# Kernel optimization log

Hardware: AMD Instinct MI355X
Metric: run time of the kernel (lower is better)

Reference implementation:

```python
import jax, jax.numpy as jnp
import numpy as np

B, LQ = 16, 2048
EMB1, EMB2, HDIM, NHEAD = 1024, 768, 1024, 16


def setup_inputs() -> dict:
    key = jax.random.key(0)
    ks = jax.random.split(key, 8)
    s1 = 1.0 / np.sqrt(EMB1)
    s2 = 1.0 / np.sqrt(EMB2)
    return {
        "emb1": jax.random.normal(ks[0], (B, LQ, EMB1), jnp.float32),
        "emb2": jax.random.normal(ks[1], (B, EMB2), jnp.float32),
        "Wq": jax.random.uniform(ks[2], (HDIM, EMB1), jnp.float32, -s1, s1),
        "bq": jax.random.uniform(ks[3], (HDIM,), jnp.float32, -s1, s1),
        "Wk": jax.random.uniform(ks[4], (HDIM, EMB2), jnp.float32, -s2, s2),
        "bk": jax.random.uniform(ks[5], (HDIM,), jnp.float32, -s2, s2),
        "Wv": jax.random.uniform(ks[6], (HDIM, EMB2), jnp.float32, -s2, s2),
        "bv": jax.random.uniform(ks[7], (HDIM,), jnp.float32, -s2, s2),
        "n_head": NHEAD,
    }


def reference(emb1, emb2, Wq, bq, Wk, bk, Wv, bv, n_head):
    b, lq, _ = emb1.shape
    hdim = Wq.shape[0]
    dh = hdim // n_head
    # Q: [b, lq, hdim] -> [b, H, lq, dh]
    q = (jnp.einsum("bqe,he->bqh", emb1, Wq) + bq).reshape(b, lq, n_head, dh).transpose(0, 2, 1, 3)
    # K, V from per-batch vector: [b, hdim] -> [b, H, 1, dh]
    k = (emb2 @ Wk.T + bk).reshape(b, 1, n_head, dh).transpose(0, 2, 1, 3)
    v = (emb2 @ Wv.T + bv).reshape(b, 1, n_head, dh).transpose(0, 2, 1, 3)
    # att: [b, H, lq, 1] (no softmax, no scaling)
    att = jnp.einsum("bhqd,bhkd->bhqk", q, k)
    # sigmoid gate broadcast-multiplied with V: [b,H,lq,1]*[b,H,1,dh] -> [b,H,lq,dh]
    out = jax.nn.sigmoid(att) * v
    # back to [b, lq, hdim]; torch .squeeze(1) is a no-op for lq > 1
    return out.transpose(0, 2, 1, 3).reshape(b, lq, hdim)
```

## Files before the change

kernel.cpp:

```cpp
#include <hip/hip_runtime.h>
#include <hip/hip_fp16.h>
#include <cstdint>


typedef float f4v __attribute__((ext_vector_type(4)));

__global__ __launch_bounds__(256) void kv_kernel(
    const float* __restrict__ emb2, const float* __restrict__ Wk,
    const float* __restrict__ bk,   const float* __restrict__ Wv,
    const float* __restrict__ bv,   float* __restrict__ ws)
{
    const int kind  = blockIdx.y;
    const int htile = blockIdx.x;
    const float* W    = kind ? Wv : Wk;
    const float* bias = kind ? bv : bk;
    float* outp = ws + (kind ? 16384 : 0);

    const int t  = threadIdx.x;
    const int es = t >> 6;
    const int hl = (t >> 4) & 3;
    const int b  = t & 15;
    const int h  = htile * 4 + hl;

    const float4* W4 = (const float4*)(W + (size_t)h * 768) + es * 48;
    const float4* E4 = (const float4*)(emb2 + (size_t)b * 768) + es * 48;

    float acc = 0.f;
    #pragma unroll 8
    for (int j = 0; j < 48; ++j) {
        float4 w = W4[j];
        float4 a = E4[j];
        acc += w.x * a.x + w.y * a.y + w.z * a.z + w.w * a.w;
    }

    __shared__ float red[256];
    red[t] = acc;
    __syncthreads();
    if (t < 64) {
        float s = red[t] + red[t + 64] + red[t + 128] + red[t + 192] + bias[h];
        outp[b * 1024 + h] = s;
    }
}

__global__ __launch_bounds__(256) void fold_kernel(
    const float* __restrict__ Wq, const float* __restrict__ bq,
    float* __restrict__ ws)
{
    const int h = blockIdx.x;
    const int b = blockIdx.y;
    const float* kvec = ws;
    float* attb = ws + 32768;
    __half* wqk = (__half*)((char*)ws + 132096);

    const int t = threadIdx.x;
    __shared__ float kk[64];
    if (t < 64) {
        float kvl = kvec[b * 1024 + h * 64 + t];
        kk[t] = kvl;
        float s = kvl * bq[h * 64 + t];
        s += __shfl_xor(s, 1);  s += __shfl_xor(s, 2);
        s += __shfl_xor(s, 4);  s += __shfl_xor(s, 8);
        s += __shfl_xor(s, 16); s += __shfl_xor(s, 32);
        if (t == 0) attb[b * 16 + h] = s;
    }
    __syncthreads();

    float4 acc = make_float4(0.f, 0.f, 0.f, 0.f);
    const float4* Wrow = (const float4*)(Wq + (size_t)(h * 64) * 1024) + t;
    #pragma unroll 8
    for (int d = 0; d < 64; ++d) {
        float4 w = Wrow[(size_t)d * 256];
        float kd = kk[d];
        acc.x += kd * w.x; acc.y += kd * w.y;
        acc.z += kd * w.z; acc.w += kd * w.w;
    }
    union { __half2 h2[2]; uint2 u; } pk;
    pk.h2[0] = __floats2half2_rn(acc.x, acc.y);
    pk.h2[1] = __floats2half2_rn(acc.z, acc.w);
    *(uint2*)(wqk + (size_t)(b * 16 + h) * 1024 + t * 4) = pk.u;
}

__global__ __launch_bounds__(256, 3) void att_kernel(
    const float* __restrict__ emb1, const float* __restrict__ ws,
    float* __restrict__ out)
{
    const int bx = blockIdx.x;
    const int b  = blockIdx.y;
    const int t    = threadIdx.x;
    const int w    = t >> 6;
    const int lane = t & 63;

    const float*  vvec = ws + 16384 + b * 1024;
    const float*  attb = ws + 32768 + b * 16;
    const __half* wqk  = (const __half*)((const char*)ws + 132096) + (size_t)b * 16384;

    float4 wf[4][4];
    #pragma unroll
    for (int hh = 0; hh < 4; ++hh) {
        const __half* wrow = wqk + (w * 4 + hh) * 1024;
        #pragma unroll
        for (int s = 0; s < 4; ++s) {
            const __half2* p = (const __half2*)(wrow + s * 256 + lane * 4);
            float2 lo = __half22float2(p[0]);
            float2 hi = __half22float2(p[1]);
            wf[hh][s] = make_float4(lo.x, lo.y, hi.x, hi.y);
        }
    }

    const int   hloc   = ((lane & 1) << 1) | ((lane >> 1) & 1);
    const float attb_l = attb[w * 4 + hloc];
    const int   gsrc   = ((lane >> 5) & 1) | (((lane >> 4) & 1) << 1);

    const float4 vv = *(const float4*)(vvec + w * 256 + lane * 4);

    const int row0 = bx * 32;
    const float* Abase = emb1 + ((size_t)b * 2048 + row0) * 1024 + lane * 4;
    float*       Obase = out  + ((size_t)b * 2048 + row0) * 1024 + w * 256 + lane * 4;

    float4 a[4], an[4];
    #pragma unroll
    for (int s = 0; s < 4; ++s) a[s] = *(const float4*)(Abase + s * 256);

    for (int r = 0; r < 32; ++r) {
        if (r < 31) {
            const float* An = Abase + (size_t)(r + 1) * 1024;
            #pragma unroll
            for (int s = 0; s < 4; ++s) an[s] = *(const float4*)(An + s * 256);
        }

        float acc[4] = {0.f, 0.f, 0.f, 0.f};
        #pragma unroll
        for (int s = 0; s < 4; ++s) {
            float4 as = a[s];
            #pragma unroll
            for (int hh = 0; hh < 4; ++hh) {
                float4 ww = wf[hh][s];
                acc[hh] += ww.x * as.x + ww.y * as.y + ww.z * as.z + ww.w * as.w;
            }
        }

        {
            const bool hi = lane & 1;
            #pragma unroll
            for (int i = 0; i < 2; ++i) {
                float send = hi ? acc[i] : acc[i + 2];
                float keep = hi ? acc[i + 2] : acc[i];
                acc[i] = keep + __shfl_xor(send, 1);
            }
        }
        float r0;
        {
            const bool hi = lane & 2;
            float send = hi ? acc[0] : acc[1];
            float keep = hi ? acc[1] : acc[0];
            r0 = keep + __shfl_xor(send, 2);
        }
        r0 += __shfl_xor(r0, 4);
        r0 += __shfl_xor(r0, 8);
        r0 += __shfl_xor(r0, 16);
        r0 += __shfl_xor(r0, 32);

        const float att  = r0 + attb_l;
        const float gate = 1.0f / (1.0f + __expf(-att));
        const float g    = __shfl(gate, gsrc);

        f4v o;
        o.x = g * vv.x; o.y = g * vv.y; o.z = g * vv.z; o.w = g * vv.w;
        __builtin_nontemporal_store(o, (f4v*)(Obase + (size_t)r * 1024));

        if (r < 31) {
            #pragma unroll
            for (int s = 0; s < 4; ++s) a[s] = an[s];
        }
    }
}

extern "C" void kernel_launch(void* const* d_in, const int* in_sizes, int n_in,
                              void* d_out, int out_size, void* d_ws, size_t ws_size,
                              hipStream_t stream) {
    const float* emb1 = (const float*)d_in[0];
    const float* emb2 = (const float*)d_in[1];
    const float* Wq   = (const float*)d_in[2];
    const float* bq   = (const float*)d_in[3];
    const float* Wk   = (const float*)d_in[4];
    const float* bk   = (const float*)d_in[5];
    const float* Wv   = (const float*)d_in[6];
    const float* bv   = (const float*)d_in[7];
    float* out = (float*)d_out;
    float* ws  = (float*)d_ws;

    kv_kernel  <<<dim3(256, 2), 256, 0, stream>>>(emb2, Wk, bk, Wv, bv, ws);
    fold_kernel<<<dim3(16, 16), 256, 0, stream>>>(Wq, bq, ws);
    att_kernel <<<dim3(64, 16), 256, 0, stream>>>(emb1, ws, out);
}
```

Baseline: 289.3 us.

## Compute the attention gate with fp16 MFMA over 16-row tiles, then broadcast through LDS

The per-row scalar dot products and shuffle reductions are replaced by a 16x16x32 fp16 MFMA per wave. Each wave computes gate logits for 16 rows by 16 heads, converting emb1 to fp16 on the fly. Gates go into shared memory, then each wave writes its 16 output rows scaled by V. This cuts ALU and shuffle work but adds fp16 rounding of activations, and the per-lane loads are less coalesced. Blocks shrink to 128 threads.

```diff
diff --git a/kernel.cpp b/kernel.cpp
--- a/kernel.cpp
+++ b/kernel.cpp
@@ -3,7 +3,8 @@
 #include <cstdint>
 
 
-typedef float f4v __attribute__((ext_vector_type(4)));
+typedef float    f4v __attribute__((ext_vector_type(4)));
+typedef _Float16 h8v __attribute__((ext_vector_type(8)));
 
 __global__ __launch_bounds__(256) void kv_kernel(
     const float* __restrict__ emb2, const float* __restrict__ Wk,
@@ -80,97 +81,75 @@
     *(uint2*)(wqk + (size_t)(b * 16 + h) * 1024 + t * 4) = pk.u;
 }
 
-__global__ __launch_bounds__(256, 3) void att_kernel(
+__global__ __launch_bounds__(128) void att_kernel(
     const float* __restrict__ emb1, const float* __restrict__ ws,
     float* __restrict__ out)
 {
-    const int bx = blockIdx.x;
-    const int b  = blockIdx.y;
+    const int b    = blockIdx.y;
     const int t    = threadIdx.x;
     const int w    = t >> 6;
     const int lane = t & 63;
+    const int q    = lane >> 4;
+    const int m    = lane & 15;
 
-    const float*  vvec = ws + 16384 + b * 1024;
-    const float*  attb = ws + 32768 + b * 16;
-    const __half* wqk  = (const __half*)((const char*)ws + 132096) + (size_t)b * 16384;
+    const int row0 = blockIdx.x * 32 + w * 16;
 
-    float4 wf[4][4];
+    const float*    vvec  = ws + 16384 + b * 1024;
+    const float*    attbp = ws + 32768 + b * 16;
+    const _Float16* wqk   = (const _Float16*)((const char*)ws + 132096)
+                          + (size_t)b * 16384;
+
+    const float*    Ap = emb1 + ((size_t)b * 2048 + row0 + m) * 1024 + q * 8;
+    const _Float16* Bp = wqk + m * 1024 + q * 8;
+
+    f4v acc = {0.f, 0.f, 0.f, 0.f};
+
+    f4v a0 = *(const f4v*)(Ap);
+    f4v a1 = *(const f4v*)(Ap + 4);
+    h8v bf = *(const h8v*)(Bp);
+
+    for (int c = 0; c < 32; ++c) {
+        const int cn = (c < 31) ? c + 1 : 31;
+        const float* An = Ap + cn * 32;
+        f4v a0n = *(const f4v*)(An);
+        f4v a1n = *(const f4v*)(An + 4);
+        h8v bfn = *(const h8v*)(Bp + cn * 32);
+
+        h8v af;
+        af[0] = (_Float16)a0[0]; af[1] = (_Float16)a0[1];
+        af[2] = (_Float16)a0[2]; af[3] = (_Float16)a0[3];
+        af[4] = (_Float16)a1[0]; af[5] = (_Float16)a1[1];
+        af[6] = (_Float16)a1[2]; af[7] = (_Float16)a1[3];
+
+        acc = __builtin_amdgcn_mfma_f32_16x16x32_f16(af, bf, acc, 0, 0, 0);
+
+        a0 = a0n; a1 = a1n; bf = bfn;
+    }
+
+    __shared__ float gl[2][16 * 17];
+    float* g = gl[w];
+    const float attb_l = attbp[m];
     #pragma unroll
-    for (int hh = 0; hh < 4; ++hh) {
-        const __half* wrow = wqk + (w * 4 + hh) * 1024;
+    for (int j = 0; j < 4; ++j) {
+        float att  = acc[j] + attb_l;
+        float gate = 1.0f / (1.0f + __expf(-att));
+        g[(q * 4 + j) * 17 + m] = gate;
+    }
+    __syncthreads();
+
+    f4v vv[4];
+    #pragma unroll
+    for (int s = 0; s < 4; ++s)
+        vv[s] = *(const f4v*)(vvec + s * 256 + lane * 4);
+
+    float* Ob = out + ((size_t)b * 2048 + row0) * 1024 + lane * 4;
+    #pragma unroll
+    for (int r = 0; r < 16; ++r) {
         #pragma unroll
         for (int s = 0; s < 4; ++s) {
-            const __half2* p = (const __half2*)(wrow + s * 256 + lane * 4);
-            float2 lo = __half22float2(p[0]);
-            float2 hi = __half22float2(p[1]);
-            wf[hh][s] = make_float4(lo.x, lo.y, hi.x, hi.y);
-        }
-    }
-
-    const int   hloc   = ((lane & 1) << 1) | ((lane >> 1) & 1);
-    const float attb_l = attb[w * 4 + hloc];
-    const int   gsrc   = ((lane >> 5) & 1) | (((lane >> 4) & 1) << 1);
-
-    const float4 vv = *(const float4*)(vvec + w * 256 + lane * 4);
-
-    const int row0 = bx * 32;
-    const float* Abase = emb1 + ((size_t)b * 2048 + row0) * 1024 + lane * 4;
-    float*       Obase = out  + ((size_t)b * 2048 + row0) * 1024 + w * 256 + lane * 4;
-
-    float4 a[4], an[4];
-    #pragma unroll
-    for (int s = 0; s < 4; ++s) a[s] = *(const float4*)(Abase + s * 256);
-
-    for (int r = 0; r < 32; ++r) {
-        if (r < 31) {
-            const float* An = Abase + (size_t)(r + 1) * 1024;
-            #pragma unroll
-            for (int s = 0; s < 4; ++s) an[s] = *(const float4*)(An + s * 256);
-        }
-
-        float acc[4] = {0.f, 0.f, 0.f, 0.f};
-        #pragma unroll
-        for (int s = 0; s < 4; ++s) {
-            float4 as = a[s];
-            #pragma unroll
-            for (int hh = 0; hh < 4; ++hh) {
-                float4 ww = wf[hh][s];
-                acc[hh] += ww.x * as.x + ww.y * as.y + ww.z * as.z + ww.w * as.w;
-            }
-        }
-
-        {
-            const bool hi = lane & 1;
-            #pragma unroll
-            for (int i = 0; i < 2; ++i) {
-                float send = hi ? acc[i] : acc[i + 2];
-                float keep = hi ? acc[i + 2] : acc[i];
-                acc[i] = keep + __shfl_xor(send, 1);
-            }
-        }
-        float r0;
-        {
-            const bool hi = lane & 2;
-            float send = hi ? acc[0] : acc[1];
-            float keep = hi ? acc[1] : acc[0];
-            r0 = keep + __shfl_xor(send, 2);
-        }
-        r0 += __shfl_xor(r0, 4);
-        r0 += __shfl_xor(r0, 8);
-        r0 += __shfl_xor(r0, 16);
-        r0 += __shfl_xor(r0, 32);
-
-        const float att  = r0 + attb_l;
-        const float gate = 1.0f / (1.0f + __expf(-att));
-        const float g    = __shfl(gate, gsrc);
-
-        f4v o;
-        o.x = g * vv.x; o.y = g * vv.y; o.z = g * vv.z; o.w = g * vv.w;
-        __builtin_nontemporal_store(o, (f4v*)(Obase + (size_t)r * 1024));
-
-        if (r < 31) {
-            #pragma unroll
-            for (int s = 0; s < 4; ++s) a[s] = an[s];
+            float gg = g[r * 17 + s * 4 + q];
+            f4v o = gg * vv[s];
+            __builtin_nontemporal_store(o, (f4v*)(Ob + (size_t)r * 1024 + s * 256));
         }
     }
 }
@@ -191,5 +170,5 @@
 
     kv_kernel  <<<dim3(256, 2), 256, 0, stream>>>(emb2, Wk, bk, Wv, bv, ws);
     fold_kernel<<<dim3(16, 16), 256, 0, stream>>>(Wq, bq, ws);
-    att_kernel <<<dim3(64, 16), 256, 0, stream>>>(emb1, ws, out);
+    att_kernel <<<dim3(64, 16), 128, 0, stream>>>(emb1, ws, out);
 }
```

New measurement: 285.3 us. Within noise of the previous version (-1.4%).
